# Optimization experiments

Measured on AMD Instinct MI355X. Metric: run time of the kernel, lower is better.

Reference implementation:

```python
import jax, jax.numpy as jnp
import numpy as np

N = 20000   # nodes
E = 320000  # edges
F = 64      # input node features
H = 256     # hidden_layer_size
C = 10      # nbr_classes
G = 64      # graphs in the batch


def _lin(key, fan_in, fan_out):
    k1, k2 = jax.random.split(key)
    bound = 1.0 / np.sqrt(fan_in)
    W = jax.random.uniform(k1, (fan_in, fan_out), jnp.float32, -bound, bound)
    b = jax.random.uniform(k2, (fan_out,), jnp.float32, -bound, bound)
    return W, b


def setup_inputs() -> dict:
    key = jax.random.key(0)
    ks = jax.random.split(key, 10)
    x = jax.random.normal(ks[0], (N, F), jnp.float32)
    edge_index = jax.random.randint(ks[1], (2, E), 0, N)
    batch = jnp.sort(jax.random.randint(ks[2], (N,), 0, G))
    W1, b1 = _lin(ks[3], F, H)
    W2, b2 = _lin(ks[4], H, H)
    W3, b3 = _lin(ks[5], H, H)
    W4, b4 = _lin(ks[6], H, H)
    W5, b5 = _lin(ks[7], H, H)
    Wout, bout = _lin(ks[8], H, C)
    return {"x": x, "edge_index": edge_index, "batch": batch,
            "W1": W1, "b1": b1, "W2": W2, "b2": b2, "W3": W3, "b3": b3,
            "W4": W4, "b4": b4, "W5": W5, "b5": b5, "Wout": Wout, "bout": bout}


def reference(x, edge_index, batch, W1, b1, W2, b2, W3, b3, W4, b4, W5, b5, Wout, bout):
    # GCNConv (Kipf & Welling): add self-loops, D^{-1/2}(A+I)D^{-1/2} (X W) + b.
    # Dropout(p=0.5) is identity in eval mode (reference is deterministic).
    loop = jnp.arange(N)
    row = jnp.concatenate([edge_index[0], loop])  # source nodes, [E+N]
    col = jnp.concatenate([edge_index[1], loop])  # target nodes, [E+N]
    deg = jax.ops.segment_sum(jnp.ones(E + N, x.dtype), col, num_segments=N)
    dinv = jax.lax.rsqrt(deg)  # deg >= 1 thanks to self-loops
    norm = (dinv[row] * dinv[col])[:, None]  # [E+N, 1]

    def gcn_conv(h, W, b):
        m = (h @ W)[row] * norm                      # gather + normalize, [E+N, H]
        return jax.ops.segment_sum(m, col, num_segments=N) + b

    h = x
    for W, b in ((W1, b1), (W2, b2), (W3, b3), (W4, b4), (W5, b5)):
        h = jax.nn.relu(gcn_conv(h, W, b))

    # global_mean_pool over graph ids
    counts = jax.ops.segment_sum(jnp.ones(N, h.dtype), batch, num_segments=G)
    pooled = jax.ops.segment_sum(h, batch, num_segments=G) / jnp.maximum(counts, 1.0)[:, None]
    return pooled @ Wout + bout  # [G, C]
```

## Files before the change

kernel.cpp:

```cpp
#include <hip/hip_runtime.h>

#define NN 20000
#define NE 320000
#define FIN 64
#define HD 256
#define NC 10
#define NG 64
#define NB ((NN + 255) / 256)
#define EBMAX (NE + 15 * NN + 16)

typedef unsigned short u16;
typedef unsigned int u32;
typedef __attribute__((ext_vector_type(8))) short short8;
typedef __attribute__((ext_vector_type(4))) float f32x4;

__device__ __forceinline__ float bf2f(u16 u) {
    union { u32 i; float f; } v; v.i = ((u32)u) << 16; return v.f;
}
__device__ __forceinline__ u16 f2bf(float f) {
    union { float f; u32 i; } v; v.f = f;
    u32 r = v.i + 0x7fffu + ((v.i >> 16) & 1u);
    return (u16)(r >> 16);
}

__global__ void k_deg(const int* __restrict__ col, int* __restrict__ degi,
                      const int* __restrict__ batch, int* __restrict__ gstart) {
    int i = blockIdx.x * 256 + threadIdx.x;
    if (i < NE) atomicAdd(&degi[col[i]], 1);
    if (i < NN) {
        int b = batch[i];
        int prev = (i == 0) ? -1 : batch[i - 1];
        if (b != prev) gstart[b] = i;
    }
}

__global__ void k_pad(u32* __restrict__ ebuf32) {
    int i = blockIdx.x * 256 + threadIdx.x;
    if (i < EBMAX / 2) ebuf32[i] = 0x4E204E20u;
}

__global__ __launch_bounds__(256) void k_scan1(const int* __restrict__ degi,
                                               int* __restrict__ rowptr,
                                               int* __restrict__ bsum) {
    int t = threadIdx.x;
    int i = blockIdx.x * 256 + t;
    int v = (i < NN) ? ((degi[i] + 15) & ~15) : 0;
    int lane = t & 63, wid = t >> 6;
    int x = v;
#pragma unroll
    for (int off = 1; off < 64; off <<= 1) {
        int y = __shfl_up(x, off);
        if (lane >= off) x += y;
    }
    __shared__ int ws[4];
    if (lane == 63) ws[wid] = x;
    __syncthreads();
    int woff = 0;
    for (int w = 0; w < wid; ++w) woff += ws[w];
    if (i < NN) rowptr[i] = woff + x - v;
    if (t == 255) bsum[blockIdx.x] = woff + x;
}

__global__ void k_scan3(const int* __restrict__ degi, const int* __restrict__ bsum,
                        int* __restrict__ rowptr, int* __restrict__ cursor,
                        float* __restrict__ dinv,
                        const float* __restrict__ x, u16* __restrict__ u0) {
    __shared__ int pref[NB];
    if (threadIdx.x < NB) pref[threadIdx.x] = bsum[threadIdx.x];
    __syncthreads();
    if (threadIdx.x == 0) {
        int run = 0;
        for (int k = 0; k < NB; ++k) { int t = pref[k]; pref[k] = run; run += t; }
    }
    __syncthreads();
    int i = blockIdx.x * 256 + threadIdx.x;
    if (i < NN) {
        int dg = degi[i];
        int rp = rowptr[i] + pref[i >> 8];
        rowptr[i] = rp;
        cursor[i] = rp;
        dinv[i] = rsqrtf((float)(1 + dg));
        if (i == NN - 1) rowptr[NN] = rp + ((dg + 15) & ~15);
    }
    if (i < NN * FIN / 4) {
        int node = i >> 4;
        float d = rsqrtf((float)(1 + degi[node]));
        float4 v = *(const float4*)&x[(size_t)i * 4];
        u32 lo = (u32)f2bf(v.x * d) | ((u32)f2bf(v.y * d) << 16);
        u32 hi = (u32)f2bf(v.z * d) | ((u32)f2bf(v.w * d) << 16);
        *(uint2*)&u0[(size_t)i * 4] = make_uint2(lo, hi);
    }
    if (blockIdx.x == 0 && threadIdx.x < FIN) u0[(size_t)NN * FIN + threadIdx.x] = 0;
}

__global__ void k_fill(const int* __restrict__ row, const int* __restrict__ col,
                       int* __restrict__ cursor, u16* __restrict__ ebuf) {
    int e = blockIdx.x * 256 + threadIdx.x;
    if (e < NE) {
        int c = col[e];
        int pos = atomicAdd(&cursor[c], 1);
        ebuf[pos] = (u16)row[e];
    }
}

__global__ __launch_bounds__(256) void k_trans(const float* __restrict__ W0, const float* __restrict__ W1,
                                               const float* __restrict__ W2, const float* __restrict__ W3,
                                               const float* __restrict__ W4,
                                               u16* __restrict__ T0, u16* __restrict__ T1,
                                               u16* __restrict__ T2, u16* __restrict__ T3,
                                               u16* __restrict__ T4) {
    int l = blockIdx.z;
    const float* W = (l == 0) ? W0 : (l == 1) ? W1 : (l == 2) ? W2 : (l == 3) ? W3 : W4;
    u16* T = (l == 0) ? T0 : (l == 1) ? T1 : (l == 2) ? T2 : (l == 3) ? T3 : T4;
    int K = (l == 0) ? FIN : HD;
    int k0 = blockIdx.x * 32;
    if (k0 >= K) return;
    int n0 = blockIdx.y * 32;
    __shared__ float tile[32][33];
    int tx = threadIdx.x & 31, ty = threadIdx.x >> 5;
#pragma unroll
    for (int r = 0; r < 32; r += 8)
        tile[ty + r][tx] = W[(size_t)(k0 + ty + r) * HD + n0 + tx];
    __syncthreads();
#pragma unroll
    for (int r = 0; r < 32; r += 8)
        T[(size_t)(n0 + ty + r) * K + k0 + tx] = f2bf(tile[tx][ty + r]);
}

__global__ __launch_bounds__(256, 3) void k_fused(const u16* __restrict__ U,
                                                  const int* __restrict__ rowptr,
                                                  const u16* __restrict__ ebuf,
                                                  const float* __restrict__ dinv,
                                                  const u16* __restrict__ Wt,
                                                  const float* __restrict__ bias,
                                                  u16* __restrict__ O,
                                                  int K, int scaleOut) {
    __shared__ u16 Asm[32][264];
    __shared__ u16 Bsm[256][40];
    __shared__ float bs[HD];
    const int m0 = blockIdx.x * 32;
    const int t = threadIdx.x;
    const int wave = t >> 6;
    const int lane = t & 63;
    bs[t] = bias[t];
    if (blockIdx.x == 0) O[(size_t)NN * HD + t] = 0;

    if (K == HD) {
        const int grp = lane >> 4;
        const int seg = lane & 15;
        for (int task = wave; task < 64; task += 4) {
            const int row = task >> 1;
            const int n = m0 + row;
            const int fbase = (task & 1) * 128 + seg * 8;
            const int s = rowptr[n], e = rowptr[n + 1];
            float acc[8];
            if (grp == 0) {
                uint4 v = *(const uint4*)&U[(size_t)n * HD + fbase];
                acc[0] = bf2f((u16)(v.x & 0xffff)); acc[1] = bf2f((u16)(v.x >> 16));
                acc[2] = bf2f((u16)(v.y & 0xffff)); acc[3] = bf2f((u16)(v.y >> 16));
                acc[4] = bf2f((u16)(v.z & 0xffff)); acc[5] = bf2f((u16)(v.z >> 16));
                acc[6] = bf2f((u16)(v.w & 0xffff)); acc[7] = bf2f((u16)(v.w >> 16));
            } else {
#pragma unroll
                for (int k = 0; k < 8; ++k) acc[k] = 0.f;
            }
            for (int j = s; j < e; j += 16) {
                int myid = (lane < 16) ? (int)ebuf[j + lane] : 0;
                uint4 v[4];
#pragma unroll
                for (int k = 0; k < 4; ++k) {
                    int r = __shfl(myid, grp * 4 + k);
                    v[k] = *(const uint4*)&U[(size_t)r * HD + fbase];
                }
#pragma unroll
                for (int k = 0; k < 4; ++k) {
                    acc[0] += bf2f((u16)(v[k].x & 0xffff)); acc[1] += bf2f((u16)(v[k].x >> 16));
                    acc[2] += bf2f((u16)(v[k].y & 0xffff)); acc[3] += bf2f((u16)(v[k].y >> 16));
                    acc[4] += bf2f((u16)(v[k].z & 0xffff)); acc[5] += bf2f((u16)(v[k].z >> 16));
                    acc[6] += bf2f((u16)(v[k].w & 0xffff)); acc[7] += bf2f((u16)(v[k].w >> 16));
                }
            }
#pragma unroll
            for (int k = 0; k < 8; ++k) {
                acc[k] += __shfl_xor(acc[k], 16);
                acc[k] += __shfl_xor(acc[k], 32);
            }
            if (grp == 0) {
                float d = dinv[n];
                uint4 o;
                o.x = (u32)f2bf(acc[0] * d) | ((u32)f2bf(acc[1] * d) << 16);
                o.y = (u32)f2bf(acc[2] * d) | ((u32)f2bf(acc[3] * d) << 16);
                o.z = (u32)f2bf(acc[4] * d) | ((u32)f2bf(acc[5] * d) << 16);
                o.w = (u32)f2bf(acc[6] * d) | ((u32)f2bf(acc[7] * d) << 16);
                *(uint4*)&Asm[row][fbase] = o;
            }
        }
    } else {
        const int grp = lane >> 3;
        const int seg = lane & 7;
        for (int task = wave; task < 32; task += 4) {
            const int n = m0 + task;
            const int s = rowptr[n], e = rowptr[n + 1];
            float acc[8];
            if (grp == 0) {
                uint4 v = *(const uint4*)&U[(size_t)n * FIN + seg * 8];
                acc[0] = bf2f((u16)(v.x & 0xffff)); acc[1] = bf2f((u16)(v.x >> 16));
                acc[2] = bf2f((u16)(v.y & 0xffff)); acc[3] = bf2f((u16)(v.y >> 16));
                acc[4] = bf2f((u16)(v.z & 0xffff)); acc[5] = bf2f((u16)(v.z >> 16));
                acc[6] = bf2f((u16)(v.w & 0xffff)); acc[7] = bf2f((u16)(v.w >> 16));
            } else {
#pragma unroll
                for (int k = 0; k < 8; ++k) acc[k] = 0.f;
            }
            for (int j = s; j < e; j += 16) {
                int r0 = (int)ebuf[j + grp];
                int r1 = (int)ebuf[j + 8 + grp];
                uint4 v0 = *(const uint4*)&U[(size_t)r0 * FIN + seg * 8];
                uint4 v1 = *(const uint4*)&U[(size_t)r1 * FIN + seg * 8];
                acc[0] += bf2f((u16)(v0.x & 0xffff)); acc[1] += bf2f((u16)(v0.x >> 16));
                acc[2] += bf2f((u16)(v0.y & 0xffff)); acc[3] += bf2f((u16)(v0.y >> 16));
                acc[4] += bf2f((u16)(v0.z & 0xffff)); acc[5] += bf2f((u16)(v0.z >> 16));
                acc[6] += bf2f((u16)(v0.w & 0xffff)); acc[7] += bf2f((u16)(v0.w >> 16));
                acc[0] += bf2f((u16)(v1.x & 0xffff)); acc[1] += bf2f((u16)(v1.x >> 16));
                acc[2] += bf2f((u16)(v1.y & 0xffff)); acc[3] += bf2f((u16)(v1.y >> 16));
                acc[4] += bf2f((u16)(v1.z & 0xffff)); acc[5] += bf2f((u16)(v1.z >> 16));
                acc[6] += bf2f((u16)(v1.w & 0xffff)); acc[7] += bf2f((u16)(v1.w >> 16));
            }
#pragma unroll
            for (int off = 8; off < 64; off <<= 1)
#pragma unroll
                for (int k = 0; k < 8; ++k) acc[k] += __shfl_xor(acc[k], off);
            if (grp == 0) {
                float d = dinv[n];
                uint4 o;
                o.x = (u32)f2bf(acc[0] * d) | ((u32)f2bf(acc[1] * d) << 16);
                o.y = (u32)f2bf(acc[2] * d) | ((u32)f2bf(acc[3] * d) << 16);
                o.z = (u32)f2bf(acc[4] * d) | ((u32)f2bf(acc[5] * d) << 16);
                o.w = (u32)f2bf(acc[6] * d) | ((u32)f2bf(acc[7] * d) << 16);
                *(uint4*)&Asm[task][seg * 8] = o;
            }
        }
    }
    __syncthreads();

    const int quad = lane >> 4;
    const int l16 = lane & 15;
    const int n0 = wave * 64;
    f32x4 acc[2][4];
#pragma unroll
    for (int i = 0; i < 2; ++i)
#pragma unroll
        for (int j = 0; j < 4; ++j) acc[i][j] = (f32x4){0.f, 0.f, 0.f, 0.f};

    for (int k0 = 0; k0 < K; k0 += 32) {
#pragma unroll
        for (int j = 0; j < 4; ++j) {
            float4 v = *(const float4*)&Wt[(size_t)t * K + k0 + j * 8];
            *(float4*)&Bsm[t][j * 8] = v;
        }
        __syncthreads();
        short8 a[2], b[4];
#pragma unroll
        for (int i = 0; i < 2; ++i) a[i] = *(const short8*)&Asm[i * 16 + l16][k0 + quad * 8];
#pragma unroll
        for (int j = 0; j < 4; ++j) b[j] = *(const short8*)&Bsm[n0 + j * 16 + l16][quad * 8];
#pragma unroll
        for (int i = 0; i < 2; ++i)
#pragma unroll
            for (int j = 0; j < 4; ++j)
                acc[i][j] = __builtin_amdgcn_mfma_f32_16x16x32_bf16(a[i], b[j], acc[i][j], 0, 0, 0);
        __syncthreads();
    }
#pragma unroll
    for (int i = 0; i < 2; ++i) {
#pragma unroll
        for (int r = 0; r < 4; ++r) {
            int m = m0 + i * 16 + quad * 4 + r;
            float d = scaleOut ? dinv[m] : 1.0f;
#pragma unroll
            for (int j = 0; j < 4; ++j) {
                int n = n0 + j * 16 + l16;
                float val = fmaxf(acc[i][j][r] + bs[n], 0.f) * d;
                O[(size_t)m * HD + n] = f2bf(val);
            }
        }
    }
}

__global__ __launch_bounds__(256) void k_poolout(const u16* __restrict__ h,
                                                 const int* __restrict__ gstart,
                                                 const float* __restrict__ Wout,
                                                 const float* __restrict__ bout,
                                                 float* __restrict__ out) {
    int g = blockIdx.x;
    int t = threadIdx.x;
    __shared__ float pooled[HD];
    __shared__ float part[NC][16];
    __shared__ int s_se[2];
    if (t == 0) {
        int st = gstart[g];
        int en = NN;
        for (int gg = g + 1; gg < NG; ++gg) en = min(en, gstart[gg]);
        s_se[0] = st; s_se[1] = en;
    }
    __syncthreads();
    int st = s_se[0], en = s_se[1];
    float a0 = 0.f, a1 = 0.f, a2 = 0.f, a3 = 0.f;
    int n = st;
    for (; n + 4 <= en; n += 4) {
        a0 += bf2f(h[(size_t)n * HD + t]);
        a1 += bf2f(h[(size_t)(n + 1) * HD + t]);
        a2 += bf2f(h[(size_t)(n + 2) * HD + t]);
        a3 += bf2f(h[(size_t)(n + 3) * HD + t]);
    }
    for (; n < en; ++n) a0 += bf2f(h[(size_t)n * HD + t]);
    float inv = 1.0f / (float)max(en - st, 1);
    pooled[t] = (a0 + a1 + a2 + a3) * inv;
    __syncthreads();
    if (t < NC * 16) {
        int c = t >> 4, l16 = t & 15;
        float s = 0.f;
        for (int f = l16; f < HD; f += 16)
            s = fmaf(pooled[f], Wout[(size_t)f * NC + c], s);
        part[c][l16] = s;
    }
    __syncthreads();
    if (t < NC) {
        float s = 0.f;
#pragma unroll
        for (int k = 0; k < 16; ++k) s += part[t][k];
        out[(size_t)g * NC + t] = s + bout[t];
    }
}

extern "C" void kernel_launch(void* const* d_in, const int* in_sizes, int n_in,
                              void* d_out, int out_size, void* d_ws, size_t ws_size,
                              hipStream_t stream) {
    const float* x     = (const float*)d_in[0];
    const int*   ei    = (const int*)d_in[1];
    const int*   batch = (const int*)d_in[2];
    const float* Wl[5] = {(const float*)d_in[3], (const float*)d_in[5], (const float*)d_in[7],
                          (const float*)d_in[9], (const float*)d_in[11]};
    const float* bl[5] = {(const float*)d_in[4], (const float*)d_in[6], (const float*)d_in[8],
                          (const float*)d_in[10], (const float*)d_in[12]};
    const float* Wout = (const float*)d_in[13];
    const float* bout = (const float*)d_in[14];
    float* out = (float*)d_out;

    const int* row = ei;
    const int* col = ei + NE;

    char* p = (char*)d_ws;
    auto take = [&](size_t bytes) { char* q = p; p += (bytes + 255) & ~(size_t)255; return q; };
    float* dinv   = (float*)take(NN * 4);
    int*   degi   = (int*)take(NN * 4);
    int*   rowptr = (int*)take((NN + 1) * 4);
    int*   cursor = (int*)take(NN * 4);
    int*   bsum   = (int*)take(NB * 4);
    u16*   ebuf   = (u16*)take(EBMAX * 2);
    int*   gstart = (int*)take(NG * 4);
    u16*   Wt[5];
    for (int l = 0; l < 5; ++l) Wt[l] = (u16*)take((size_t)HD * HD * 2);
    u16*   B1     = (u16*)take((size_t)(NN + 1) * HD * 2);
    u16*   B2     = (u16*)take((size_t)(NN + 1) * HD * 2);

    hipMemsetAsync(degi, 0, NN * 4, stream);
    hipMemsetAsync(gstart, 0x7F, NG * 4, stream);
    k_deg<<<(NE + 255) / 256, 256, 0, stream>>>(col, degi, batch, gstart);
    k_pad<<<(EBMAX / 2 + 255) / 256, 256, 0, stream>>>((u32*)ebuf);
    k_scan1<<<NB, 256, 0, stream>>>(degi, rowptr, bsum);
    k_scan3<<<(NN * FIN / 4 + 255) / 256, 256, 0, stream>>>(degi, bsum, rowptr, cursor, dinv, x, B1);
    k_fill<<<(NE + 255) / 256, 256, 0, stream>>>(row, col, cursor, ebuf);
    dim3 tGrid(8, 8, 5);
    k_trans<<<tGrid, 256, 0, stream>>>(Wl[0], Wl[1], Wl[2], Wl[3], Wl[4],
                                       Wt[0], Wt[1], Wt[2], Wt[3], Wt[4]);

    const int fGrid = NN / 32;
    k_fused<<<fGrid, 256, 0, stream>>>(B1, rowptr, ebuf, dinv, Wt[0], bl[0], B2, FIN, 1);
    k_fused<<<fGrid, 256, 0, stream>>>(B2, rowptr, ebuf, dinv, Wt[1], bl[1], B1, HD, 1);
    k_fused<<<fGrid, 256, 0, stream>>>(B1, rowptr, ebuf, dinv, Wt[2], bl[2], B2, HD, 1);
    k_fused<<<fGrid, 256, 0, stream>>>(B2, rowptr, ebuf, dinv, Wt[3], bl[3], B1, HD, 1);
    k_fused<<<fGrid, 256, 0, stream>>>(B1, rowptr, ebuf, dinv, Wt[4], bl[4], B2, HD, 0);

    k_poolout<<<NG, 256, 0, stream>>>(B2, gstart, Wout, bout, out);
}
```

Baseline: 395.7 us.

## Shrink fused GCN tile to 16 rows with 512-thread blocks

The fused aggregate+GEMM kernel now handles 16 nodes per block with 8 waves instead of 32 nodes with 4 waves. Each wave computes a 16x32 output slice, and the weight tile load is split across twice as many threads. The goal is more blocks and more waves in flight to hide gather latency, with fewer accumulator registers per thread. In exchange, the weight tile is reloaded from global memory for every 16 nodes, doubling that traffic, and each wave issues fewer MFMAs per barrier.

```diff
diff --git a/kernel.cpp b/kernel.cpp
--- a/kernel.cpp
+++ b/kernel.cpp
@@ -127,7 +127,7 @@
         T[(size_t)(n0 + ty + r) * K + k0 + tx] = f2bf(tile[tx][ty + r]);
 }
 
-__global__ __launch_bounds__(256, 3) void k_fused(const u16* __restrict__ U,
+__global__ __launch_bounds__(512, 8) void k_fused(const u16* __restrict__ U,
                                                   const int* __restrict__ rowptr,
                                                   const u16* __restrict__ ebuf,
                                                   const float* __restrict__ dinv,
@@ -135,20 +135,20 @@
                                                   const float* __restrict__ bias,
                                                   u16* __restrict__ O,
                                                   int K, int scaleOut) {
-    __shared__ u16 Asm[32][264];
+    __shared__ u16 Asm[16][264];
     __shared__ u16 Bsm[256][40];
     __shared__ float bs[HD];
-    const int m0 = blockIdx.x * 32;
+    const int m0 = blockIdx.x * 16;
     const int t = threadIdx.x;
     const int wave = t >> 6;
     const int lane = t & 63;
-    bs[t] = bias[t];
-    if (blockIdx.x == 0) O[(size_t)NN * HD + t] = 0;
+    if (t < HD) bs[t] = bias[t];
+    if (blockIdx.x == 0 && t < HD) O[(size_t)NN * HD + t] = 0;
 
     if (K == HD) {
         const int grp = lane >> 4;
         const int seg = lane & 15;
-        for (int task = wave; task < 64; task += 4) {
+        for (int task = wave; task < 32; task += 8) {
             const int row = task >> 1;
             const int n = m0 + row;
             const int fbase = (task & 1) * 128 + seg * 8;
@@ -198,7 +198,7 @@
     } else {
         const int grp = lane >> 3;
         const int seg = lane & 7;
-        for (int task = wave; task < 32; task += 4) {
+        for (int task = wave; task < 16; task += 8) {
             const int n = m0 + task;
             const int s = rowptr[n], e = rowptr[n + 1];
             float acc[8];
@@ -245,44 +245,39 @@
 
     const int quad = lane >> 4;
     const int l16 = lane & 15;
-    const int n0 = wave * 64;
-    f32x4 acc[2][4];
-#pragma unroll
-    for (int i = 0; i < 2; ++i)
-#pragma unroll
-        for (int j = 0; j < 4; ++j) acc[i][j] = (f32x4){0.f, 0.f, 0.f, 0.f};
+    const int n0 = wave * 32;
+    f32x4 acc[2];
+#pragma unroll
+    for (int j = 0; j < 2; ++j) acc[j] = (f32x4){0.f, 0.f, 0.f, 0.f};
 
     for (int k0 = 0; k0 < K; k0 += 32) {
-#pragma unroll
-        for (int j = 0; j < 4; ++j) {
-            float4 v = *(const float4*)&Wt[(size_t)t * K + k0 + j * 8];
-            *(float4*)&Bsm[t][j * 8] = v;
+        {
+            int r = t >> 1, h16 = (t & 1) * 16;
+#pragma unroll
+            for (int j = 0; j < 2; ++j) {
+                float4 v = *(const float4*)&Wt[(size_t)r * K + k0 + h16 + j * 8];
+                *(float4*)&Bsm[r][h16 + j * 8] = v;
+            }
         }
         __syncthreads();
-        short8 a[2], b[4];
-#pragma unroll
-        for (int i = 0; i < 2; ++i) a[i] = *(const short8*)&Asm[i * 16 + l16][k0 + quad * 8];
-#pragma unroll
-        for (int j = 0; j < 4; ++j) b[j] = *(const short8*)&Bsm[n0 + j * 16 + l16][quad * 8];
-#pragma unroll
-        for (int i = 0; i < 2; ++i)
-#pragma unroll
-            for (int j = 0; j < 4; ++j)
-                acc[i][j] = __builtin_amdgcn_mfma_f32_16x16x32_bf16(a[i], b[j], acc[i][j], 0, 0, 0);
+        short8 a = *(const short8*)&Asm[l16][k0 + quad * 8];
+        short8 b[2];
+#pragma unroll
+        for (int j = 0; j < 2; ++j) b[j] = *(const short8*)&Bsm[n0 + j * 16 + l16][quad * 8];
+#pragma unroll
+        for (int j = 0; j < 2; ++j)
+            acc[j] = __builtin_amdgcn_mfma_f32_16x16x32_bf16(a, b[j], acc[j], 0, 0, 0);
         __syncthreads();
     }
 #pragma unroll
-    for (int i = 0; i < 2; ++i) {
-#pragma unroll
-        for (int r = 0; r < 4; ++r) {
-            int m = m0 + i * 16 + quad * 4 + r;
-            float d = scaleOut ? dinv[m] : 1.0f;
-#pragma unroll
-            for (int j = 0; j < 4; ++j) {
-                int n = n0 + j * 16 + l16;
-                float val = fmaxf(acc[i][j][r] + bs[n], 0.f) * d;
-                O[(size_t)m * HD + n] = f2bf(val);
-            }
+    for (int r = 0; r < 4; ++r) {
+        int m = m0 + quad * 4 + r;
+        float d = scaleOut ? dinv[m] : 1.0f;
+#pragma unroll
+        for (int j = 0; j < 2; ++j) {
+            int n = n0 + j * 16 + l16;
+            float val = fmaxf(acc[j][r] + bs[n], 0.f) * d;
+            O[(size_t)m * HD + n] = f2bf(val);
         }
     }
 }
@@ -375,12 +370,12 @@
     k_trans<<<tGrid, 256, 0, stream>>>(Wl[0], Wl[1], Wl[2], Wl[3], Wl[4],
                                        Wt[0], Wt[1], Wt[2], Wt[3], Wt[4]);
 
-    const int fGrid = NN / 32;
-    k_fused<<<fGrid, 256, 0, stream>>>(B1, rowptr, ebuf, dinv, Wt[0], bl[0], B2, FIN, 1);
-    k_fused<<<fGrid, 256, 0, stream>>>(B2, rowptr, ebuf, dinv, Wt[1], bl[1], B1, HD, 1);
-    k_fused<<<fGrid, 256, 0, stream>>>(B1, rowptr, ebuf, dinv, Wt[2], bl[2], B2, HD, 1);
-    k_fused<<<fGrid, 256, 0, stream>>>(B2, rowptr, ebuf, dinv, Wt[3], bl[3], B1, HD, 1);
-    k_fused<<<fGrid, 256, 0, stream>>>(B1, rowptr, ebuf, dinv, Wt[4], bl[4], B2, HD, 0);
+    const int fGrid = NN / 16;
+    k_fused<<<fGrid, 512, 0, stream>>>(B1, rowptr, ebuf, dinv, Wt[0], bl[0], B2, FIN, 1);
+    k_fused<<<fGrid, 512, 0, stream>>>(B2, rowptr, ebuf, dinv, Wt[1], bl[1], B1, HD, 1);
+    k_fused<<<fGrid, 512, 0, stream>>>(B1, rowptr, ebuf, dinv, Wt[2], bl[2], B2, HD, 1);
+    k_fused<<<fGrid, 512, 0, stream>>>(B2, rowptr, ebuf, dinv, Wt[3], bl[3], B1, HD, 1);
+    k_fused<<<fGrid, 512, 0, stream>>>(B1, rowptr, ebuf, dinv, Wt[4], bl[4], B2, HD, 0);
 
     k_poolout<<<NG, 256, 0, stream>>>(B2, gstart, Wout, bout, out);
 }
```

Result: faster. 333.5 us (-15.7%).
